# Performance work log

Hardware: AMD Instinct MI355X
Metric: run time of the kernel (lower is better)

## Reference

```python
import jax, jax.numpy as jnp
import numpy as np

B, T, I, H, O = 64, 512, 512, 1024, 1


def setup_inputs() -> dict:
    key = jax.random.key(0)
    ks = jax.random.split(key, 12)
    s_i = 1.0 / np.sqrt(H)  # torch LSTM init scale ~ U(-1/sqrt(H), 1/sqrt(H)); normal*scale is fine for a numeric baseline
    return {
        "x": jax.random.normal(ks[0], (B, T, I), dtype=jnp.float32),
        "W_ih0": jax.random.normal(ks[1], (4 * H, I), dtype=jnp.float32) * s_i,
        "W_hh0": jax.random.normal(ks[2], (4 * H, H), dtype=jnp.float32) * s_i,
        "b_ih0": jax.random.normal(ks[3], (4 * H,), dtype=jnp.float32) * s_i,
        "b_hh0": jax.random.normal(ks[4], (4 * H,), dtype=jnp.float32) * s_i,
        "W_ih1": jax.random.normal(ks[5], (4 * H, H), dtype=jnp.float32) * s_i,
        "W_hh1": jax.random.normal(ks[6], (4 * H, H), dtype=jnp.float32) * s_i,
        "b_ih1": jax.random.normal(ks[7], (4 * H,), dtype=jnp.float32) * s_i,
        "b_hh1": jax.random.normal(ks[8], (4 * H,), dtype=jnp.float32) * s_i,
        "W_out": jax.random.normal(ks[9], (O, H), dtype=jnp.float32) * s_i,
        "b_out": jax.random.normal(ks[10], (O,), dtype=jnp.float32) * s_i,
    }


def _lstm_layer(x, W_ih, W_hh, b_ih, b_hh):
    # x: [B, T, D_in] -> h_seq: [B, T, H]. Gate order (i, f, g, o) as in torch.
    h_dim = W_hh.shape[1]
    batch = x.shape[0]
    # Precompute input contribution for all timesteps: [B, T, 4H]
    gx = jnp.einsum("btd,gd->btg", x, W_ih) + b_ih + b_hh
    gx_t = jnp.swapaxes(gx, 0, 1)  # [T, B, 4H]

    def step(carry, g_in):
        h, c = carry
        gates = g_in + h @ W_hh.T  # [B, 4H]
        i, f, g, o = jnp.split(gates, 4, axis=-1)
        i = jax.nn.sigmoid(i)
        f = jax.nn.sigmoid(f)
        g = jnp.tanh(g)
        o = jax.nn.sigmoid(o)
        c = f * c + i * g
        h = o * jnp.tanh(c)
        return (h, c), h

    h0 = jnp.zeros((batch, h_dim), dtype=x.dtype)
    c0 = jnp.zeros((batch, h_dim), dtype=x.dtype)
    _, hs = jax.lax.scan(step, (h0, c0), gx_t)  # hs: [T, B, H]
    return jnp.swapaxes(hs, 0, 1)


def reference(x, W_ih0, W_hh0, b_ih0, b_hh0, W_ih1, W_hh1, b_ih1, b_hh1, W_out, b_out):
    h1 = _lstm_layer(x, W_ih0, W_hh0, b_ih0, b_hh0)   # layer 0 (dropout=0.0 between layers)
    h2 = _lstm_layer(h1, W_ih1, W_hh1, b_ih1, b_hh1)  # layer 1
    last = h2[:, -1, :]                               # [B, H]
    out = last @ W_out.T + b_out                      # [B, O]
    return jax.nn.sigmoid(out)                        # sigmoid=True
```

## Files before the change

### kernel.cpp

```cpp
#include <hip/hip_runtime.h>
#include <hip/hip_bf16.h>


namespace {

constexpr int B_ = 64, T_ = 512, I_ = 512, H_ = 1024;
constexpr int NWG = 256, NTHR = 256;
constexpr int BH = B_ * H_;

typedef __attribute__((ext_vector_type(8))) short short8;
typedef __attribute__((ext_vector_type(4))) float f32x4;

#define MFMA16(a, b, c) __builtin_amdgcn_mfma_f32_16x16x32_bf16((a), (b), (c), 0, 0, 0)

__device__ __forceinline__ float sigm(float x)  { return 1.f / (1.f + __expf(-x)); }
__device__ __forceinline__ float tanhx(float x) { return 2.f / (1.f + __expf(-2.f * x)) - 1.f; }

__device__ __forceinline__ unsigned f2bf(float f) {
  unsigned u = __float_as_uint(f);
  unsigned rnd = 0x7FFFu + ((u >> 16) & 1u);
  return (u + rnd) >> 16;
}
__device__ __forceinline__ float bf2f(unsigned short s) {
  return __uint_as_float(((unsigned)s) << 16);
}

__global__ void cvt_bf16_k(const float* __restrict__ src, unsigned short* __restrict__ dst, int n4) {
  int i = blockIdx.x * 256 + threadIdx.x;
  if (i >= n4) return;
  float4 v = reinterpret_cast<const float4*>(src)[i];
  ushort4 o;
  o.x = (unsigned short)f2bf(v.x); o.y = (unsigned short)f2bf(v.y);
  o.z = (unsigned short)f2bf(v.z); o.w = (unsigned short)f2bf(v.w);
  reinterpret_cast<ushort4*>(dst)[i] = o;
}

__global__ void zero_init_k(unsigned short* __restrict__ h1, unsigned short* __restrict__ h2,
                            unsigned* __restrict__ bar) {
  int i = blockIdx.x * 256 + threadIdx.x;
  if (i < BH) h1[(size_t)T_ * BH + i] = 0;
  if (i < BH) h2[(size_t)T_ * BH + i] = 0;
  if (i < 2048) bar[i] = 0;
}

__global__ __launch_bounds__(NTHR, 1) void lstm_fused(
    const unsigned short* __restrict__ xb,
    const unsigned short* __restrict__ wih0, const unsigned short* __restrict__ whh0,
    const float* __restrict__ bih0, const float* __restrict__ bhh0,
    const unsigned short* __restrict__ wih1, const unsigned short* __restrict__ whh1,
    const float* __restrict__ bih1, const float* __restrict__ bhh1,
    unsigned short* __restrict__ h1rec, unsigned short* __restrict__ h2rec,
    unsigned* __restrict__ bars)
{
  __shared__ unsigned short s_win[32768];
  __shared__ unsigned short s_whh[32768];

  const int tid   = threadIdx.x;
  const int wg    = blockIdx.x;
  const int layer = wg >> 7;
  const int lwg   = wg & 127;
  const int wave  = tid >> 6;
  const int lane  = tid & 63;
  const int j0    = lwg * 8;
  const int n     = lane & 15;
  const int u4    = lane >> 4;
  const int k0    = u4 * 8;
  const int arow  = wave * 16 + n;

  const unsigned short* w_in = layer ? wih1 : wih0;
  const unsigned short* w_hh = layer ? whh1 : whh0;
  const float* b_i = layer ? bih1 : bih0;
  const float* b_h = layer ? bhh1 : bhh0;
  unsigned short* rec = layer ? h2rec : h1rec;
  const int K_IN = layer ? 1024 : 512;
  const int NKI  = K_IN / 32;

  unsigned* grp = bars + (wg >> 3) * 32;
  unsigned* rel = bars + 1024 + (wg & 7) * 32;

  for (int c = tid; c < 2 * NKI * 64; c += NTHR) {
    int l  = c & 63;
    int kk = (c >> 6) % NKI;
    int rt = c / (NKI * 64);
    int rr = l & 15, q = l >> 4;
    int grow = (rr & 3) * H_ + j0 + rt * 4 + (rr >> 2);
    *reinterpret_cast<short8*>(&s_win[c * 8]) =
        *reinterpret_cast<const short8*>(&w_in[(size_t)grow * K_IN + kk * 32 + q * 8]);
  }
  for (int c = tid; c < 2 * 32 * 64; c += NTHR) {
    int l  = c & 63;
    int kk = (c >> 6) & 31;
    int rt = c >> 11;
    int rr = l & 15, q = l >> 4;
    int grow = (rr & 3) * H_ + j0 + rt * 4 + (rr >> 2);
    *reinterpret_cast<short8*>(&s_whh[c * 8]) =
        *reinterpret_cast<const short8*>(&w_hh[(size_t)grow * H_ + kk * 32 + q * 8]);
  }
  float bias0[4], bias1[4];
  #pragma unroll
  for (int g = 0; g < 4; ++g) {
    bias0[g] = b_i[g * H_ + j0 + u4]     + b_h[g * H_ + j0 + u4];
    bias1[g] = b_i[g * H_ + j0 + 4 + u4] + b_h[g * H_ + j0 + 4 + u4];
  }
  __syncthreads();

  float cst0 = 0.f, cst1 = 0.f;
  f32x4 na0 = {0.f, 0.f, 0.f, 0.f}, na1 = {0.f, 0.f, 0.f, 0.f};

  if (layer == 0) {
    const unsigned short* a_in = xb + (size_t)arow * (T_ * I_) + k0;
    #pragma unroll
    for (int kk = 0; kk < 16; ++kk) {
      short8 bv = *reinterpret_cast<const short8*>(a_in + kk * 32);
      na0 = MFMA16(*reinterpret_cast<const short8*>(&s_win[(kk * 64 + lane) * 8]),          bv, na0);
      na1 = MFMA16(*reinterpret_cast<const short8*>(&s_win[((16 + kk) * 64 + lane) * 8]),   bv, na1);
    }
  }

  for (int p = 0; p <= T_ + 1; ++p) {
    if (p > 0) {
      const unsigned tgt = (unsigned)p * 8u;
      if (wg < 8) {
        if (wave == 0) {
          for (;;) {
            unsigned v = 0xFFFFFFFFu;
            if (lane < 32)
              v = __hip_atomic_load(bars + lane * 32, __ATOMIC_RELAXED, __HIP_MEMORY_SCOPE_AGENT);
            if (__all((int)(lane >= 32 || v >= tgt))) break;
            __builtin_amdgcn_s_sleep(1);
          }
          if (lane == 0)
            __hip_atomic_store(rel, (unsigned)p, __ATOMIC_RELAXED, __HIP_MEMORY_SCOPE_AGENT);
        } else {
          while (__hip_atomic_load(rel, __ATOMIC_RELAXED, __HIP_MEMORY_SCOPE_AGENT) < (unsigned)p)
            __builtin_amdgcn_s_sleep(1);
        }
      } else {
        while (__hip_atomic_load(rel, __ATOMIC_RELAXED, __HIP_MEMORY_SCOPE_AGENT) < (unsigned)p)
          __builtin_amdgcn_s_sleep(1);
      }
      __builtin_amdgcn_fence(__ATOMIC_ACQUIRE, "workgroup");
    }

    f32x4 acc0 = na0, acc1 = na1;
    const int t = layer ? p - 2 : p;

    if (t >= 0 && t < T_) {
      const unsigned short* a_h = rec + (size_t)(T_ - t) * BH + (size_t)arow * H_ + k0;
      short8 hf[32];
      #pragma unroll
      for (int kk = 0; kk < 32; ++kk)
        hf[kk] = *reinterpret_cast<const short8*>(a_h + kk * 32);
      #pragma unroll
      for (int kk = 0; kk < 32; ++kk) {
        acc0 = MFMA16(*reinterpret_cast<const short8*>(&s_whh[(kk * 64 + lane) * 8]),        hf[kk], acc0);
        acc1 = MFMA16(*reinterpret_cast<const short8*>(&s_whh[((32 + kk) * 64 + lane) * 8]), hf[kk], acc1);
      }

      float gi0 = sigm(acc0[0] + bias0[0]);
      float gf0 = sigm(acc0[1] + bias0[1]);
      float gg0 = tanhx(acc0[2] + bias0[2]);
      float go0 = sigm(acc0[3] + bias0[3]);
      cst0 = gf0 * cst0 + gi0 * gg0;
      float hv0 = go0 * tanhx(cst0);

      float gi1 = sigm(acc1[0] + bias1[0]);
      float gf1 = sigm(acc1[1] + bias1[1]);
      float gg1 = tanhx(acc1[2] + bias1[2]);
      float go1 = sigm(acc1[3] + bias1[3]);
      cst1 = gf1 * cst1 + gi1 * gg1;
      float hv1 = go1 * tanhx(cst1);

      unsigned a16 = f2bf(hv0) & 0xFFFFu;
      unsigned b16 = f2bf(hv1) & 0xFFFFu;
      unsigned a1 = __shfl(a16, (lane & 15) | 16, 64);
      unsigned a2 = __shfl(a16, (lane & 15) | 32, 64);
      unsigned a3 = __shfl(a16, (lane & 15) | 48, 64);
      unsigned b1 = __shfl(b16, (lane & 15) | 16, 64);
      unsigned b2 = __shfl(b16, (lane & 15) | 32, 64);
      unsigned b3 = __shfl(b16, (lane & 15) | 48, 64);
      if (lane < 16) {
        unsigned long long qa = (unsigned long long)(a16 | (a1 << 16)) |
                                ((unsigned long long)(a2 | (a3 << 16)) << 32);
        unsigned long long qb = (unsigned long long)(b16 | (b1 << 16)) |
                                ((unsigned long long)(b2 | (b3 << 16)) << 32);
        unsigned long long* dst = (unsigned long long*)
            (rec + (size_t)(T_ - t - 1) * BH + (size_t)(wave * 16 + lane) * H_ + j0);
        __hip_atomic_store(dst,     qa, __ATOMIC_RELAXED, __HIP_MEMORY_SCOPE_AGENT);
        __hip_atomic_store(dst + 1, qb, __ATOMIC_RELAXED, __HIP_MEMORY_SCOPE_AGENT);
      }
    }

    __syncthreads();
    if (tid == 0)
      __hip_atomic_fetch_add(grp, 1u, __ATOMIC_RELAXED, __HIP_MEMORY_SCOPE_AGENT);

    na0 = (f32x4){0.f, 0.f, 0.f, 0.f};
    na1 = (f32x4){0.f, 0.f, 0.f, 0.f};
    const int tn = layer ? p - 1 : p + 1;
    if (tn >= 0 && tn < T_) {
      if (layer == 0) {
        const unsigned short* a_in = xb + (size_t)arow * (T_ * I_) + (size_t)tn * I_ + k0;
        #pragma unroll
        for (int kk = 0; kk < 16; ++kk) {
          short8 bv = *reinterpret_cast<const short8*>(a_in + kk * 32);
          na0 = MFMA16(*reinterpret_cast<const short8*>(&s_win[(kk * 64 + lane) * 8]),        bv, na0);
          na1 = MFMA16(*reinterpret_cast<const short8*>(&s_win[((16 + kk) * 64 + lane) * 8]), bv, na1);
        }
      } else {
        const unsigned short* a_in = h1rec + (size_t)(T_ - 1 - tn) * BH + (size_t)arow * H_ + k0;
        #pragma unroll
        for (int kk = 0; kk < 32; ++kk) {
          short8 bv = *reinterpret_cast<const short8*>(a_in + kk * 32);
          na0 = MFMA16(*reinterpret_cast<const short8*>(&s_win[(kk * 64 + lane) * 8]),        bv, na0);
          na1 = MFMA16(*reinterpret_cast<const short8*>(&s_win[((32 + kk) * 64 + lane) * 8]), bv, na1);
        }
      }
    }
  }
}

__global__ void out_head(const unsigned short* __restrict__ h2,
                         const float* __restrict__ W_out,
                         const float* __restrict__ b_out,
                         float* __restrict__ out) {
  int b = blockIdx.x;
  int lane = threadIdx.x;
  float s = 0.f;
  for (int k = lane; k < H_; k += 64)
    s += bf2f(h2[(size_t)b * H_ + k]) * W_out[k];
  #pragma unroll
  for (int off = 32; off; off >>= 1) s += __shfl_down(s, off, 64);
  if (lane == 0) out[b] = sigm(s + b_out[0]);
}

}

extern "C" void kernel_launch(void* const* d_in, const int* in_sizes, int n_in,
                              void* d_out, int out_size, void* d_ws, size_t ws_size,
                              hipStream_t stream) {
  const float* x    = (const float*)d_in[0];
  const float* Wih0 = (const float*)d_in[1];
  const float* Whh0 = (const float*)d_in[2];
  const float* bih0 = (const float*)d_in[3];
  const float* bhh0 = (const float*)d_in[4];
  const float* Wih1 = (const float*)d_in[5];
  const float* Whh1 = (const float*)d_in[6];
  const float* bih1 = (const float*)d_in[7];
  const float* bhh1 = (const float*)d_in[8];
  const float* Wout = (const float*)d_in[9];
  const float* bout = (const float*)d_in[10];
  float* out = (float*)d_out;

  char* ws = (char*)d_ws;
  size_t off = 0;
  auto alloc = [&](size_t bytes) -> char* {
    char* p = ws + off;
    off += (bytes + 4095) & ~(size_t)4095;
    return p;
  };
  const size_t REC = (size_t)(T_ + 1) * BH * 2;

  unsigned* bar        = (unsigned*)alloc(8192);
  unsigned short* xb   = (unsigned short*)alloc((size_t)B_ * T_ * I_ * 2);
  unsigned short* wih0 = (unsigned short*)alloc((size_t)4 * H_ * I_ * 2);
  unsigned short* whh0 = (unsigned short*)alloc((size_t)4 * H_ * H_ * 2);
  unsigned short* wih1 = (unsigned short*)alloc((size_t)4 * H_ * H_ * 2);
  unsigned short* whh1 = (unsigned short*)alloc((size_t)4 * H_ * H_ * 2);
  unsigned short* h1   = (unsigned short*)alloc(REC);
  unsigned short* h2   = (unsigned short*)alloc(REC);

  auto cvt = [&](const float* s, unsigned short* d, int nelem) {
    int n4 = nelem / 4;
    cvt_bf16_k<<<(n4 + 255) / 256, 256, 0, stream>>>(s, d, n4);
  };
  cvt(x,    xb,   B_ * T_ * I_);
  cvt(Wih0, wih0, 4 * H_ * I_);
  cvt(Whh0, whh0, 4 * H_ * H_);
  cvt(Wih1, wih1, 4 * H_ * H_);
  cvt(Whh1, whh1, 4 * H_ * H_);
  zero_init_k<<<(BH + 255) / 256, 256, 0, stream>>>(h1, h2, bar);

  lstm_fused<<<NWG, NTHR, 0, stream>>>(
      xb, wih0, whh0, bih0, bhh0, wih1, whh1, bih1, bhh1, h1, h2, bar);

  out_head<<<B_, 64, 0, stream>>>(h2, Wout, bout, out);
}
```

Before: 4.271 ms.

## Merge input and recurrent weights into one LDS block and compute gates in-step

Combines the input and recurrent weight tiles into a single shared-memory array and computes the full gate pre-activation (input plus recurrent terms) inside each timestep after the barrier. This removes the post-barrier prefetch of the next step's input projection and loads all activation fragments up front in one batch. In exchange, the input-projection MFMAs now sit on the serial critical path between barriers rather than overlapping with the wait, and the larger register fragment arrays raise register pressure.

```diff
diff --git a/kernel.cpp b/kernel.cpp
--- a/kernel.cpp
+++ b/kernel.cpp
@@ -52,8 +52,7 @@
     unsigned short* __restrict__ h1rec, unsigned short* __restrict__ h2rec,
     unsigned* __restrict__ bars)
 {
-  __shared__ unsigned short s_win[32768];
-  __shared__ unsigned short s_whh[32768];
+  __shared__ unsigned short s_w[65536];
 
   const int tid   = threadIdx.x;
   const int wg    = blockIdx.x;
@@ -62,39 +61,32 @@
   const int wave  = tid >> 6;
   const int lane  = tid & 63;
   const int j0    = lwg * 8;
-  const int n     = lane & 15;
   const int u4    = lane >> 4;
   const int k0    = u4 * 8;
-  const int arow  = wave * 16 + n;
-
-  const unsigned short* w_in = layer ? wih1 : wih0;
-  const unsigned short* w_hh = layer ? whh1 : whh0;
+  const int arow  = wave * 16 + (lane & 15);
+
   const float* b_i = layer ? bih1 : bih0;
   const float* b_h = layer ? bhh1 : bhh0;
   unsigned short* rec = layer ? h2rec : h1rec;
-  const int K_IN = layer ? 1024 : 512;
-  const int NKI  = K_IN / 32;
+  const int NKT = layer ? 64 : 48;
 
   unsigned* grp = bars + (wg >> 3) * 32;
   unsigned* rel = bars + 1024 + (wg & 7) * 32;
 
-  for (int c = tid; c < 2 * NKI * 64; c += NTHR) {
-    int l  = c & 63;
-    int kk = (c >> 6) % NKI;
-    int rt = c / (NKI * 64);
-    int rr = l & 15, q = l >> 4;
+  for (int c = tid; c < 2 * NKT * 64; c += NTHR) {
+    int l   = c & 63;
+    int kkt = (c >> 6) % NKT;
+    int rt  = c / (NKT * 64);
+    int rr  = l & 15, q = l >> 4;
     int grow = (rr & 3) * H_ + j0 + rt * 4 + (rr >> 2);
-    *reinterpret_cast<short8*>(&s_win[c * 8]) =
-        *reinterpret_cast<const short8*>(&w_in[(size_t)grow * K_IN + kk * 32 + q * 8]);
-  }
-  for (int c = tid; c < 2 * 32 * 64; c += NTHR) {
-    int l  = c & 63;
-    int kk = (c >> 6) & 31;
-    int rt = c >> 11;
-    int rr = l & 15, q = l >> 4;
-    int grow = (rr & 3) * H_ + j0 + rt * 4 + (rr >> 2);
-    *reinterpret_cast<short8*>(&s_whh[c * 8]) =
-        *reinterpret_cast<const short8*>(&w_hh[(size_t)grow * H_ + kk * 32 + q * 8]);
+    const unsigned short* src;
+    if (layer == 0)
+      src = (kkt < 16) ? &wih0[(size_t)grow * 512 + kkt * 32 + q * 8]
+                       : &whh0[(size_t)grow * 1024 + (kkt - 16) * 32 + q * 8];
+    else
+      src = (kkt < 32) ? &wih1[(size_t)grow * 1024 + kkt * 32 + q * 8]
+                       : &whh1[(size_t)grow * 1024 + (kkt - 32) * 32 + q * 8];
+    *reinterpret_cast<short8*>(&s_w[c * 8]) = *reinterpret_cast<const short8*>(src);
   }
   float bias0[4], bias1[4];
   #pragma unroll
@@ -105,17 +97,6 @@
   __syncthreads();
 
   float cst0 = 0.f, cst1 = 0.f;
-  f32x4 na0 = {0.f, 0.f, 0.f, 0.f}, na1 = {0.f, 0.f, 0.f, 0.f};
-
-  if (layer == 0) {
-    const unsigned short* a_in = xb + (size_t)arow * (T_ * I_) + k0;
-    #pragma unroll
-    for (int kk = 0; kk < 16; ++kk) {
-      short8 bv = *reinterpret_cast<const short8*>(a_in + kk * 32);
-      na0 = MFMA16(*reinterpret_cast<const short8*>(&s_win[(kk * 64 + lane) * 8]),          bv, na0);
-      na1 = MFMA16(*reinterpret_cast<const short8*>(&s_win[((16 + kk) * 64 + lane) * 8]),   bv, na1);
-    }
-  }
 
   for (int p = 0; p <= T_ + 1; ++p) {
     if (p > 0) {
@@ -142,19 +123,41 @@
       __builtin_amdgcn_fence(__ATOMIC_ACQUIRE, "workgroup");
     }
 
-    f32x4 acc0 = na0, acc1 = na1;
     const int t = layer ? p - 2 : p;
 
     if (t >= 0 && t < T_) {
-      const unsigned short* a_h = rec + (size_t)(T_ - t) * BH + (size_t)arow * H_ + k0;
-      short8 hf[32];
-      #pragma unroll
-      for (int kk = 0; kk < 32; ++kk)
-        hf[kk] = *reinterpret_cast<const short8*>(a_h + kk * 32);
-      #pragma unroll
-      for (int kk = 0; kk < 32; ++kk) {
-        acc0 = MFMA16(*reinterpret_cast<const short8*>(&s_whh[(kk * 64 + lane) * 8]),        hf[kk], acc0);
-        acc1 = MFMA16(*reinterpret_cast<const short8*>(&s_whh[((32 + kk) * 64 + lane) * 8]), hf[kk], acc1);
+      f32x4 acc0 = {0.f, 0.f, 0.f, 0.f}, acc1 = {0.f, 0.f, 0.f, 0.f};
+
+      if (layer == 0) {
+        const unsigned short* xr = xb + (size_t)arow * (T_ * I_) + (size_t)t * I_ + k0;
+        const unsigned short* hr = h1rec + (size_t)(T_ - t) * BH + (size_t)arow * H_ + k0;
+        short8 bf[48];
+        #pragma unroll
+        for (int kk = 0; kk < 16; ++kk)
+          bf[kk] = *reinterpret_cast<const short8*>(xr + kk * 32);
+        #pragma unroll
+        for (int kk = 0; kk < 32; ++kk)
+          bf[16 + kk] = *reinterpret_cast<const short8*>(hr + kk * 32);
+        #pragma unroll
+        for (int kk = 0; kk < 48; ++kk) {
+          acc0 = MFMA16(*reinterpret_cast<const short8*>(&s_w[(kk * 64 + lane) * 8]),        bf[kk], acc0);
+          acc1 = MFMA16(*reinterpret_cast<const short8*>(&s_w[((48 + kk) * 64 + lane) * 8]), bf[kk], acc1);
+        }
+      } else {
+        const unsigned short* ar = h1rec + (size_t)(T_ - t - 1) * BH + (size_t)arow * H_ + k0;
+        const unsigned short* hr = h2rec + (size_t)(T_ - t) * BH + (size_t)arow * H_ + k0;
+        short8 bf[64];
+        #pragma unroll
+        for (int kk = 0; kk < 32; ++kk)
+          bf[kk] = *reinterpret_cast<const short8*>(ar + kk * 32);
+        #pragma unroll
+        for (int kk = 0; kk < 32; ++kk)
+          bf[32 + kk] = *reinterpret_cast<const short8*>(hr + kk * 32);
+        #pragma unroll
+        for (int kk = 0; kk < 64; ++kk) {
+          acc0 = MFMA16(*reinterpret_cast<const short8*>(&s_w[(kk * 64 + lane) * 8]),        bf[kk], acc0);
+          acc1 = MFMA16(*reinterpret_cast<const short8*>(&s_w[((64 + kk) * 64 + lane) * 8]), bf[kk], acc1);
+        }
       }
 
       float gi0 = sigm(acc0[0] + bias0[0]);
@@ -194,29 +197,6 @@
     __syncthreads();
     if (tid == 0)
       __hip_atomic_fetch_add(grp, 1u, __ATOMIC_RELAXED, __HIP_MEMORY_SCOPE_AGENT);
-
-    na0 = (f32x4){0.f, 0.f, 0.f, 0.f};
-    na1 = (f32x4){0.f, 0.f, 0.f, 0.f};
-    const int tn = layer ? p - 1 : p + 1;
-    if (tn >= 0 && tn < T_) {
-      if (layer == 0) {
-        const unsigned short* a_in = xb + (size_t)arow * (T_ * I_) + (size_t)tn * I_ + k0;
-        #pragma unroll
-        for (int kk = 0; kk < 16; ++kk) {
-          short8 bv = *reinterpret_cast<const short8*>(a_in + kk * 32);
-          na0 = MFMA16(*reinterpret_cast<const short8*>(&s_win[(kk * 64 + lane) * 8]),        bv, na0);
-          na1 = MFMA16(*reinterpret_cast<const short8*>(&s_win[((16 + kk) * 64 + lane) * 8]), bv, na1);
-        }
-      } else {
-        const unsigned short* a_in = h1rec + (size_t)(T_ - 1 - tn) * BH + (size_t)arow * H_ + k0;
-        #pragma unroll
-        for (int kk = 0; kk < 32; ++kk) {
-          short8 bv = *reinterpret_cast<const short8*>(a_in + kk * 32);
-          na0 = MFMA16(*reinterpret_cast<const short8*>(&s_win[(kk * 64 + lane) * 8]),        bv, na0);
-          na1 = MFMA16(*reinterpret_cast<const short8*>(&s_win[((32 + kk) * 64 + lane) * 8]), bv, na1);
-        }
-      }
-    }
   }
 }
 
```

Result: slower. 5.829 ms (+36.5%).

## Decouple layer barriers so each LSTM layer syncs independently with layer-1 polling layer-0 progress

Applied to the files above, without the earlier changes.

Replaces the single global barrier over all 256 workgroups with two independent per-layer barriers of 128 workgroups each. Layer 1 no longer runs in lockstep two steps behind layer 0. Before consuming layer-0's h for a step, each layer-1 wave polls layer-0's group counters directly. This is meant to cut barrier fan-in and let layer 0 run ahead without waiting on layer 1, at the cost of extra per-wave polling traffic in layer 1.

```diff
diff --git a/kernel.cpp b/kernel.cpp
--- a/kernel.cpp
+++ b/kernel.cpp
@@ -62,10 +62,10 @@
   const int wave  = tid >> 6;
   const int lane  = tid & 63;
   const int j0    = lwg * 8;
-  const int n     = lane & 15;
   const int u4    = lane >> 4;
   const int k0    = u4 * 8;
-  const int arow  = wave * 16 + n;
+  const int arow  = wave * 16 + (lane & 15);
+  const int lbase = layer * 16;
 
   const unsigned short* w_in = layer ? wih1 : wih0;
   const unsigned short* w_hh = layer ? whh1 : whh0;
@@ -75,8 +75,8 @@
   const int K_IN = layer ? 1024 : 512;
   const int NKI  = K_IN / 32;
 
-  unsigned* grp = bars + (wg >> 3) * 32;
-  unsigned* rel = bars + 1024 + (wg & 7) * 32;
+  unsigned* grp = bars + (lbase + (lwg >> 3)) * 32;
+  unsigned* rel = bars + 1024 + (layer * 8 + (lwg & 7)) * 32;
 
   for (int c = tid; c < 2 * NKI * 64; c += NTHR) {
     int l  = c & 63;
@@ -112,40 +112,54 @@
     #pragma unroll
     for (int kk = 0; kk < 16; ++kk) {
       short8 bv = *reinterpret_cast<const short8*>(a_in + kk * 32);
-      na0 = MFMA16(*reinterpret_cast<const short8*>(&s_win[(kk * 64 + lane) * 8]),          bv, na0);
-      na1 = MFMA16(*reinterpret_cast<const short8*>(&s_win[((16 + kk) * 64 + lane) * 8]),   bv, na1);
-    }
-  }
-
-  for (int p = 0; p <= T_ + 1; ++p) {
-    if (p > 0) {
-      const unsigned tgt = (unsigned)p * 8u;
-      if (wg < 8) {
+      na0 = MFMA16(*reinterpret_cast<const short8*>(&s_win[(kk * 64 + lane) * 8]),        bv, na0);
+      na1 = MFMA16(*reinterpret_cast<const short8*>(&s_win[((16 + kk) * 64 + lane) * 8]), bv, na1);
+    }
+  } else {
+    for (;;) {
+      unsigned v = 0xFFFFFFFFu;
+      if (lane < 16)
+        v = __hip_atomic_load(bars + lane * 32, __ATOMIC_RELAXED, __HIP_MEMORY_SCOPE_AGENT);
+      if (__all((int)(lane >= 16 || v >= 8u))) break;
+      __builtin_amdgcn_s_sleep(1);
+    }
+    __builtin_amdgcn_fence(__ATOMIC_ACQUIRE, "workgroup");
+    const unsigned short* a_in = h1rec + (size_t)(T_ - 1) * BH + (size_t)arow * H_ + k0;
+    #pragma unroll
+    for (int kk = 0; kk < 32; ++kk) {
+      short8 bv = *reinterpret_cast<const short8*>(a_in + kk * 32);
+      na0 = MFMA16(*reinterpret_cast<const short8*>(&s_win[(kk * 64 + lane) * 8]),        bv, na0);
+      na1 = MFMA16(*reinterpret_cast<const short8*>(&s_win[((32 + kk) * 64 + lane) * 8]), bv, na1);
+    }
+  }
+
+  for (int t = 0; t < T_; ++t) {
+    if (t > 0) {
+      if (lwg < 8) {
         if (wave == 0) {
+          const unsigned tgt = (unsigned)t * 8u;
           for (;;) {
             unsigned v = 0xFFFFFFFFu;
-            if (lane < 32)
-              v = __hip_atomic_load(bars + lane * 32, __ATOMIC_RELAXED, __HIP_MEMORY_SCOPE_AGENT);
-            if (__all((int)(lane >= 32 || v >= tgt))) break;
+            if (lane < 16)
+              v = __hip_atomic_load(bars + (lbase + lane) * 32, __ATOMIC_RELAXED, __HIP_MEMORY_SCOPE_AGENT);
+            if (__all((int)(lane >= 16 || v >= tgt))) break;
             __builtin_amdgcn_s_sleep(1);
           }
           if (lane == 0)
-            __hip_atomic_store(rel, (unsigned)p, __ATOMIC_RELAXED, __HIP_MEMORY_SCOPE_AGENT);
+            __hip_atomic_store(rel, (unsigned)t, __ATOMIC_RELAXED, __HIP_MEMORY_SCOPE_AGENT);
         } else {
-          while (__hip_atomic_load(rel, __ATOMIC_RELAXED, __HIP_MEMORY_SCOPE_AGENT) < (unsigned)p)
+          while (__hip_atomic_load(rel, __ATOMIC_RELAXED, __HIP_MEMORY_SCOPE_AGENT) < (unsigned)t)
             __builtin_amdgcn_s_sleep(1);
         }
       } else {
-        while (__hip_atomic_load(rel, __ATOMIC_RELAXED, __HIP_MEMORY_SCOPE_AGENT) < (unsigned)p)
+        while (__hip_atomic_load(rel, __ATOMIC_RELAXED, __HIP_MEMORY_SCOPE_AGENT) < (unsigned)t)
           __builtin_amdgcn_s_sleep(1);
       }
       __builtin_amdgcn_fence(__ATOMIC_ACQUIRE, "workgroup");
     }
 
     f32x4 acc0 = na0, acc1 = na1;
-    const int t = layer ? p - 2 : p;
-
-    if (t >= 0 && t < T_) {
+    {
       const unsigned short* a_h = rec + (size_t)(T_ - t) * BH + (size_t)arow * H_ + k0;
       short8 hf[32];
       #pragma unroll
@@ -156,39 +170,39 @@
         acc0 = MFMA16(*reinterpret_cast<const short8*>(&s_whh[(kk * 64 + lane) * 8]),        hf[kk], acc0);
         acc1 = MFMA16(*reinterpret_cast<const short8*>(&s_whh[((32 + kk) * 64 + lane) * 8]), hf[kk], acc1);
       }
-
-      float gi0 = sigm(acc0[0] + bias0[0]);
-      float gf0 = sigm(acc0[1] + bias0[1]);
-      float gg0 = tanhx(acc0[2] + bias0[2]);
-      float go0 = sigm(acc0[3] + bias0[3]);
-      cst0 = gf0 * cst0 + gi0 * gg0;
-      float hv0 = go0 * tanhx(cst0);
-
-      float gi1 = sigm(acc1[0] + bias1[0]);
-      float gf1 = sigm(acc1[1] + bias1[1]);
-      float gg1 = tanhx(acc1[2] + bias1[2]);
-      float go1 = sigm(acc1[3] + bias1[3]);
-      cst1 = gf1 * cst1 + gi1 * gg1;
-      float hv1 = go1 * tanhx(cst1);
-
-      unsigned a16 = f2bf(hv0) & 0xFFFFu;
-      unsigned b16 = f2bf(hv1) & 0xFFFFu;
-      unsigned a1 = __shfl(a16, (lane & 15) | 16, 64);
-      unsigned a2 = __shfl(a16, (lane & 15) | 32, 64);
-      unsigned a3 = __shfl(a16, (lane & 15) | 48, 64);
-      unsigned b1 = __shfl(b16, (lane & 15) | 16, 64);
-      unsigned b2 = __shfl(b16, (lane & 15) | 32, 64);
-      unsigned b3 = __shfl(b16, (lane & 15) | 48, 64);
-      if (lane < 16) {
-        unsigned long long qa = (unsigned long long)(a16 | (a1 << 16)) |
-                                ((unsigned long long)(a2 | (a3 << 16)) << 32);
-        unsigned long long qb = (unsigned long long)(b16 | (b1 << 16)) |
-                                ((unsigned long long)(b2 | (b3 << 16)) << 32);
-        unsigned long long* dst = (unsigned long long*)
-            (rec + (size_t)(T_ - t - 1) * BH + (size_t)(wave * 16 + lane) * H_ + j0);
-        __hip_atomic_store(dst,     qa, __ATOMIC_RELAXED, __HIP_MEMORY_SCOPE_AGENT);
-        __hip_atomic_store(dst + 1, qb, __ATOMIC_RELAXED, __HIP_MEMORY_SCOPE_AGENT);
-      }
+    }
+
+    float gi0 = sigm(acc0[0] + bias0[0]);
+    float gf0 = sigm(acc0[1] + bias0[1]);
+    float gg0 = tanhx(acc0[2] + bias0[2]);
+    float go0 = sigm(acc0[3] + bias0[3]);
+    cst0 = gf0 * cst0 + gi0 * gg0;
+    float hv0 = go0 * tanhx(cst0);
+
+    float gi1 = sigm(acc1[0] + bias1[0]);
+    float gf1 = sigm(acc1[1] + bias1[1]);
+    float gg1 = tanhx(acc1[2] + bias1[2]);
+    float go1 = sigm(acc1[3] + bias1[3]);
+    cst1 = gf1 * cst1 + gi1 * gg1;
+    float hv1 = go1 * tanhx(cst1);
+
+    unsigned a16 = f2bf(hv0) & 0xFFFFu;
+    unsigned b16 = f2bf(hv1) & 0xFFFFu;
+    unsigned a1 = __shfl(a16, (lane & 15) | 16, 64);
+    unsigned a2 = __shfl(a16, (lane & 15) | 32, 64);
+    unsigned a3 = __shfl(a16, (lane & 15) | 48, 64);
+    unsigned b1 = __shfl(b16, (lane & 15) | 16, 64);
+    unsigned b2 = __shfl(b16, (lane & 15) | 32, 64);
+    unsigned b3 = __shfl(b16, (lane & 15) | 48, 64);
+    if (lane < 16) {
+      unsigned long long qa = (unsigned long long)(a16 | (a1 << 16)) |
+                              ((unsigned long long)(a2 | (a3 << 16)) << 32);
+      unsigned long long qb = (unsigned long long)(b16 | (b1 << 16)) |
+                              ((unsigned long long)(b2 | (b3 << 16)) << 32);
+      unsigned long long* dst = (unsigned long long*)
+          (rec + (size_t)(T_ - t - 1) * BH + (size_t)(wave * 16 + lane) * H_ + j0);
+      __hip_atomic_store(dst,     qa, __ATOMIC_RELAXED, __HIP_MEMORY_SCOPE_AGENT);
+      __hip_atomic_store(dst + 1, qb, __ATOMIC_RELAXED, __HIP_MEMORY_SCOPE_AGENT);
     }
 
     __syncthreads();
@@ -197,8 +211,8 @@
 
     na0 = (f32x4){0.f, 0.f, 0.f, 0.f};
     na1 = (f32x4){0.f, 0.f, 0.f, 0.f};
-    const int tn = layer ? p - 1 : p + 1;
-    if (tn >= 0 && tn < T_) {
+    const int tn = t + 1;
+    if (tn < T_) {
       if (layer == 0) {
         const unsigned short* a_in = xb + (size_t)arow * (T_ * I_) + (size_t)tn * I_ + k0;
         #pragma unroll
@@ -208,6 +222,15 @@
           na1 = MFMA16(*reinterpret_cast<const short8*>(&s_win[((16 + kk) * 64 + lane) * 8]), bv, na1);
         }
       } else {
+        const unsigned tgt0 = (unsigned)(tn + 1) * 8u;
+        for (;;) {
+          unsigned v = 0xFFFFFFFFu;
+          if (lane < 16)
+            v = __hip_atomic_load(bars + lane * 32, __ATOMIC_RELAXED, __HIP_MEMORY_SCOPE_AGENT);
+          if (__all((int)(lane >= 16 || v >= tgt0))) break;
+          __builtin_amdgcn_s_sleep(1);
+        }
+        __builtin_amdgcn_fence(__ATOMIC_ACQUIRE, "workgroup");
         const unsigned short* a_in = h1rec + (size_t)(T_ - 1 - tn) * BH + (size_t)arow * H_ + k0;
         #pragma unroll
         for (int kk = 0; kk < 32; ++kk) {
```

Result: slower. 5.586 ms (+30.8%).
